# Performance work log

Hardware: AMD Instinct MI355X
Metric: run time of the kernel (lower is better)

Reference implementation:

```python
import jax, jax.numpy as jnp
import numpy as np

B, P, ENC = 64, 196, 2048          # batch, num_pixels (14x14), encoder_dim
A, E, D, V = 512, 512, 512, 20000  # attention_dim, embed_dim, decoder_dim, vocab
MAXLEN = 22
T = MAXLEN - 1                     # decode steps (teacher forcing drops last token)


def _lin(k, fan_in, fan_out, scale=0.02):
    return jax.random.normal(k, (fan_in, fan_out), jnp.float32) * scale, jnp.zeros((fan_out,), jnp.float32)


def setup_inputs() -> dict:
    key = jax.random.key(0)
    ks = jax.random.split(key, 16)
    encoder_out = jax.random.normal(ks[0], (B, P, ENC), jnp.float32)
    captions = jax.random.randint(ks[1], (B, MAXLEN), 0, V)
    lens = jax.random.randint(ks[2], (B,), 2, MAXLEN + 1)
    lens = jnp.sort(lens)[::-1].at[0].set(MAXLEN)  # sorted descending, as the torch loop assumes
    emb = jax.random.uniform(ks[3], (V, E), jnp.float32, -0.1, 0.1)
    enc_att_w, enc_att_b = _lin(ks[4], ENC, A)
    dec_att_w, dec_att_b = _lin(ks[5], D, A)
    full_att_w, full_att_b = _lin(ks[6], A, 1)
    w_ih = jax.random.normal(ks[7], (E + ENC, 4 * D), jnp.float32) * 0.02
    w_hh = jax.random.normal(ks[8], (D, 4 * D), jnp.float32) * 0.02
    b_ih = jnp.zeros((4 * D,), jnp.float32)
    b_hh = jnp.zeros((4 * D,), jnp.float32)
    init_h_w, init_h_b = _lin(ks[9], ENC, D)
    init_c_w, init_c_b = _lin(ks[10], ENC, D)
    f_beta_w, f_beta_b = _lin(ks[11], D, ENC)
    fc_w = jax.random.uniform(ks[12], (D, V), jnp.float32, -0.1, 0.1)
    fc_b = jnp.zeros((V,), jnp.float32)
    return dict(encoder_out=encoder_out, captions=captions, lengths=lens, emb=emb,
                enc_att_w=enc_att_w, enc_att_b=enc_att_b, dec_att_w=dec_att_w, dec_att_b=dec_att_b,
                full_att_w=full_att_w, full_att_b=full_att_b, w_ih=w_ih, b_ih=b_ih, w_hh=w_hh, b_hh=b_hh,
                init_h_w=init_h_w, init_h_b=init_h_b, init_c_w=init_c_w, init_c_b=init_c_b,
                f_beta_w=f_beta_w, f_beta_b=f_beta_b, fc_w=fc_w, fc_b=fc_b)


def reference(encoder_out, captions, lengths, emb,
              enc_att_w, enc_att_b, dec_att_w, dec_att_b, full_att_w, full_att_b,
              w_ih, b_ih, w_hh, b_hh, init_h_w, init_h_b, init_c_w, init_c_b,
              f_beta_w, f_beta_b, fc_w, fc_b):
    # Dropout is identity (eval mode) for a deterministic reference.
    dec_len = lengths - 1                       # decode_lengths
    x_emb = emb[captions]                       # (B, L, E)
    mean_enc = encoder_out.mean(axis=1)         # (B, ENC)
    h0 = mean_enc @ init_h_w + init_h_b         # (B, D)
    c0 = mean_enc @ init_c_w + init_c_b
    att1 = encoder_out @ enc_att_w + enc_att_b  # (B, P, A), hoisted out of the loop

    emb_ts = jnp.swapaxes(x_emb[:, :T, :], 0, 1)  # (T, B, E)
    t_idx = jnp.arange(T)

    def step(carry, xt):
        h, c = carry
        e_t, t = xt
        active = (t < dec_len)[:, None]         # ragged batch -> mask (sorted lengths)
        # Bahdanau attention
        att2 = h @ dec_att_w + dec_att_b        # (B, A)
        scores = (jax.nn.relu(att1 + att2[:, None, :]) @ full_att_w)[..., 0] + full_att_b[0]  # (B, P)
        alpha = jax.nn.softmax(scores, axis=1)
        context = jnp.einsum('bp,bpe->be', alpha, encoder_out)
        # gated context
        gate = jax.nn.sigmoid(h @ f_beta_w + f_beta_b)
        context = gate * context
        # LSTMCell (torch gate order i, f, g, o)
        x = jnp.concatenate([e_t, context], axis=1)
        gates = x @ w_ih + h @ w_hh + b_ih + b_hh
        i_g, f_g, g_g, o_g = jnp.split(gates, 4, axis=1)
        c_new = jax.nn.sigmoid(f_g) * c + jax.nn.sigmoid(i_g) * jnp.tanh(g_g)
        h_new = jax.nn.sigmoid(o_g) * jnp.tanh(c_new)
        h = jnp.where(active, h_new, h)
        c = jnp.where(active, c_new, c)
        preds = jnp.where(active, h_new @ fc_w + fc_b, 0.0)
        alpha_o = jnp.where(active, alpha, 0.0)
        return (h, c), (preds, alpha_o)

    _, (preds, alphas) = jax.lax.scan(step, (h0, c0), (emb_ts, t_idx))
    predictions = jnp.swapaxes(preds, 0, 1)     # (B, T, V)
    alphas = jnp.swapaxes(alphas, 0, 1)         # (B, T, P)
    return predictions, alphas
```

## Files before the change

kernel.cpp:

```cpp
#include <hip/hip_runtime.h>

#define BB   64
#define PP   196
#define ENC  2048
#define AA   512
#define EE   512
#define DD   512
#define VV   20000
#define TT   21
#define ML   22

#define PRED_ELEMS ((size_t)BB * TT * VV)

typedef __attribute__((ext_vector_type(8))) short s8bf;
typedef __attribute__((ext_vector_type(4))) float f4acc;

__device__ __forceinline__ float bf2f(unsigned short u) {
    union { unsigned int i; float f; } v; v.i = ((unsigned int)u) << 16; return v.f;
}
__device__ __forceinline__ void unpack2(unsigned int u, float& lo, float& hi) {
    union { unsigned int i; float f; } a, b;
    a.i = u << 16; b.i = u & 0xFFFF0000u; lo = a.f; hi = b.f;
}
__device__ __forceinline__ unsigned short f2bf(float f) {
    union { float f; unsigned int i; } v; v.f = f;
    unsigned int i = v.i;
    return (unsigned short)((i + 0x7FFFu + ((i >> 16) & 1u)) >> 16);
}
__device__ __forceinline__ float sigmoidf(float x) { return 1.0f / (1.0f + __expf(-x)); }

template <bool F> __device__ __forceinline__ float ldw(const void* p, size_t i) {
    if (F) return ((const float*)p)[i];
    return bf2f(((const unsigned short*)p)[i]);
}
template <bool F> __device__ __forceinline__ unsigned short ldbf(const void* p, size_t i) {
    if (F) return f2bf(((const float*)p)[i]);
    return ((const unsigned short*)p)[i];
}
template <bool F> __device__ __forceinline__ float2 ld2(const void* p, size_t i) {
    if (F) return *(const float2*)((const float*)p + i);
    unsigned int u = *(const unsigned int*)((const unsigned short*)p + i);
    float lo, hi; unpack2(u, lo, hi); return make_float2(lo, hi);
}
template <bool F> __device__ __forceinline__ float4 ld4(const void* p, size_t i) {
    if (F) return *(const float4*)((const float*)p + i);
    uint2 u = *(const uint2*)((const unsigned short*)p + i);
    float a, b, c, d; unpack2(u.x, a, b); unpack2(u.y, c, d);
    return make_float4(a, b, c, d);
}
template <bool F> __device__ __forceinline__ void st1(void* p, size_t i, float v) {
    if (F) ((float*)p)[i] = v; else ((unsigned short*)p)[i] = f2bf(v);
}

__global__ void dec_detect_kernel(const unsigned short* __restrict__ enc_us, int* __restrict__ flag) {
    __shared__ int s_cnt;
    if (threadIdx.x == 0) s_cnt = 0;
    __syncthreads();
    int cnt = 0;
    for (int i = threadIdx.x; i < 8192; i += 256) {
        unsigned short u = enc_us[2 * i];
        if ((u & 0x7F80) == 0x7F80) cnt++;
    }
    if (cnt) atomicAdd(&s_cnt, cnt);
    __syncthreads();
    if (threadIdx.x == 0) *flag = (s_cnt > 0) ? 1 : 0;
}

template <bool F>
__device__ __forceinline__ void encconv_body(const void* enc, unsigned short* dst) {
    size_t i = ((size_t)blockIdx.x * 256 + threadIdx.x) * 8;
    if (F) {
        const float* s = (const float*)enc + i;
        float4 v0 = *(const float4*)s, v1 = *(const float4*)(s + 4);
        union { uint4 u; unsigned short h[8]; } o;
        o.h[0]=f2bf(v0.x); o.h[1]=f2bf(v0.y); o.h[2]=f2bf(v0.z); o.h[3]=f2bf(v0.w);
        o.h[4]=f2bf(v1.x); o.h[5]=f2bf(v1.y); o.h[6]=f2bf(v1.z); o.h[7]=f2bf(v1.w);
        *(uint4*)(dst + i) = o.u;
    } else {
        *(uint4*)(dst + i) = *(const uint4*)((const unsigned short*)enc + i);
    }
}
__global__ void enc_bf_kernel(const void* __restrict__ enc, const int* __restrict__ flg,
                              unsigned short* __restrict__ dst) {
    if (*flg) encconv_body<true>(enc, dst); else encconv_body<false>(enc, dst);
}

template <bool F>
__device__ __forceinline__ void conv_swz_body(const void* W, int K, int Norig,
                                              unsigned short* dst, int permMode, int nChunks) {
    int chunk = blockIdx.x * 4 + (threadIdx.x >> 6);
    if (chunk >= nChunks) return;
    int lane = threadIdx.x & 63;
    int KC = K >> 5;
    int nt = chunk / KC, kc = chunk % KC;
    int quad = lane >> 4, l15 = lane & 15;
    int np = nt * 16 + l15;
    int col;
    if (permMode == 1) col = ((np >> 4) & 3) * 512 + (np >> 6) * 16 + (np & 15);
    else col = np;
    union { s8bf v; unsigned short s[8]; } o;
    if (np < Norig || permMode == 1) {
        size_t base = (size_t)(kc * 32 + quad * 8) * Norig + col;
#pragma unroll
        for (int j = 0; j < 8; ++j) o.s[j] = ldbf<F>(W, base + (size_t)j * Norig);
    } else {
#pragma unroll
        for (int j = 0; j < 8; ++j) o.s[j] = 0;
    }
    *(s8bf*)(dst + ((size_t)chunk * 64 + lane) * 8) = o.v;
}
__global__ void conv_swz_kernel(const int* __restrict__ flg, const void* __restrict__ W,
                                int K, int Norig, unsigned short* __restrict__ dst,
                                int permMode, int nChunks) {
    if (*flg) conv_swz_body<true>(W, K, Norig, dst, permMode, nChunks);
    else      conv_swz_body<false>(W, K, Norig, dst, permMode, nChunks);
}

template <bool F>
__device__ __forceinline__ void conv_bias_body(const void* dab, const void* fbb,
                                               const void* bih, const void* bhh, const void* fcb,
                                               const void* ihb, const void* icb, const void* eab,
                                               float* ag_b, float* g_b, float* fc_b,
                                               float* ihb_f, float* icb_f, float* eab_f) {
    int i = blockIdx.x * 256 + threadIdx.x;
    if (i < 2560) ag_b[i] = (i < 512) ? ldw<F>(dab, i) : ldw<F>(fbb, i - 512);
    else if (i < 2560 + 2048) {
        int np = i - 2560;
        int orig = ((np >> 4) & 3) * 512 + (np >> 6) * 16 + (np & 15);
        g_b[np] = ldw<F>(bih, orig) + ldw<F>(bhh, orig);
    } else if (i < 2560 + 2048 + 20000) fc_b[i - 4608] = ldw<F>(fcb, i - 4608);
    else if (i < 2560 + 2048 + 20000 + 512) ihb_f[i - 24608] = ldw<F>(ihb, i - 24608);
    else if (i < 2560 + 2048 + 20000 + 1024) icb_f[i - 25120] = ldw<F>(icb, i - 25120);
    else if (i < 2560 + 2048 + 20000 + 1536) eab_f[i - 25632] = ldw<F>(eab, i - 25632);
}
__global__ void conv_bias_kernel(const int* __restrict__ flg,
                                 const void* dab, const void* fbb, const void* bih, const void* bhh,
                                 const void* fcb, const void* ihb, const void* icb, const void* eab,
                                 float* ag_b, float* g_b, float* fc_b,
                                 float* ihb_f, float* icb_f, float* eab_f) {
    if (*flg) conv_bias_body<true>(dab, fbb, bih, bhh, fcb, ihb, icb, eab, ag_b, g_b, fc_b, ihb_f, icb_f, eab_f);
    else      conv_bias_body<false>(dab, fbb, bih, bhh, fcb, ihb, icb, eab, ag_b, g_b, fc_b, ihb_f, icb_f, eab_f);
}

template <bool F>
__device__ __forceinline__ void mean_body(const void* enc, unsigned short* mean_bf) {
    int b = blockIdx.x;
    int e = blockIdx.y * 256 + threadIdx.x;
    size_t base = (size_t)b * PP * ENC + e;
    float s = 0.f;
#pragma unroll 4
    for (int p = 0; p < PP; ++p) s += ldw<F>(enc, base + (size_t)p * ENC);
    mean_bf[b * ENC + e] = f2bf(s * (1.0f / (float)PP));
}
__global__ void dec_mean_kernel(const void* __restrict__ enc, const int* __restrict__ flg,
                                unsigned short* __restrict__ mean_bf) {
    if (*flg) mean_body<true>(enc, mean_bf); else mean_body<false>(enc, mean_bf);
}

__global__ __launch_bounds__(256)
void gemm_u_kernel(const int* __restrict__ flg,
                   const unsigned short* __restrict__ A1, int K1, const unsigned short* __restrict__ W1,
                   const unsigned short* __restrict__ A2, int K2, const unsigned short* __restrict__ W2,
                   const float* __restrict__ bias, int N, int epi, int nct,
                   float* __restrict__ outF, float* __restrict__ outF2,
                   unsigned short* __restrict__ hb, float* __restrict__ cptr,
                   unsigned short* __restrict__ h_all,
                   void* __restrict__ outV, const int* __restrict__ lengths, int t) {
    __shared__ float s_g[64 * 132];
    int tid = threadIdx.x;
    int wave = tid >> 6, lane = tid & 63;
    int l15 = lane & 15, quad = lane >> 4;
    const unsigned short* Abase1 = A1;
    if (epi == 2) Abase1 = A1 + (size_t)blockIdx.x * 64 * K1;
    f4acc acc[4][2];
#pragma unroll
    for (int a = 0; a < 4; ++a) { acc[a][0] = (f4acc)0.f; acc[a][1] = (f4acc)0.f; }
#pragma unroll
    for (int pass = 0; pass < 2; ++pass) {
        const unsigned short* A = pass ? A2 : Abase1;
        if (!A) continue;
        int K = pass ? K2 : K1;
        const unsigned short* W = pass ? W2 : W1;
        int KC = K >> 5;
        for (int kc = 0; kc < KC; ++kc) {
            s8bf af[4];
#pragma unroll
            for (int rt = 0; rt < 4; ++rt)
                af[rt] = *(const s8bf*)(A + (size_t)(rt * 16 + l15) * K + kc * 32 + quad * 8);
#pragma unroll
            for (int ct = 0; ct < 2; ++ct) if (ct < nct) {
                int nt = blockIdx.y * 4 * nct + ct * 4 + wave;
                s8bf bv = *(const s8bf*)(W + ((size_t)(nt * KC + kc) * 64 + lane) * 8);
#pragma unroll
                for (int rt = 0; rt < 4; ++rt)
                    acc[rt][ct] = __builtin_amdgcn_mfma_f32_16x16x32_bf16(af[rt], bv, acc[rt][ct], 0, 0, 0);
            }
        }
    }
    if (epi == 4) {
        int nl = wave * 16 + l15;
        int g = (nl >> 4) & 3, dl = nl & 15;
        float bv = bias[blockIdx.y * 64 + nl];
#pragma unroll
        for (int rt = 0; rt < 4; ++rt)
#pragma unroll
            for (int r = 0; r < 4; ++r) {
                int m = rt * 16 + quad * 4 + r;
                s_g[(g * 64 + m) * 17 + dl] = acc[rt][0][r] + bv;
            }
        __syncthreads();
        int m = tid >> 2;
        bool act = t < (lengths[m] - 1);
#pragma unroll
        for (int i = 0; i < 4; ++i) {
            int dl2 = (tid & 3) * 4 + i;
            int d = blockIdx.y * 16 + dl2;
            unsigned short hv;
            if (act) {
                float ig = sigmoidf(s_g[(0 * 64 + m) * 17 + dl2]);
                float fg = sigmoidf(s_g[(1 * 64 + m) * 17 + dl2]);
                float gg = tanhf(s_g[(2 * 64 + m) * 17 + dl2]);
                float og = sigmoidf(s_g[(3 * 64 + m) * 17 + dl2]);
                float cn = fg * cptr[m * DD + d] + ig * gg;
                float hn = og * tanhf(cn);
                cptr[m * DD + d] = cn;
                hv = f2bf(hn);
            } else {
                hv = A2[(size_t)m * K2 + d];
            }
            hb[m * DD + d] = hv;
            h_all[((size_t)t * BB + m) * DD + d] = hv;
        }
        return;
    }
    if (epi == 2) {
        int t2 = blockIdx.x;
        int base_n = blockIdx.y * 128;
#pragma unroll
        for (int ct = 0; ct < 2; ++ct) {
            int nl = ct * 64 + wave * 16 + l15;
            int nn = base_n + nl;
            float bv = (nn < VV) ? bias[nn] : 0.f;
#pragma unroll
            for (int rt = 0; rt < 4; ++rt)
#pragma unroll
                for (int r = 0; r < 4; ++r) {
                    int m = rt * 16 + quad * 4 + r;
                    s_g[m * 132 + nl] = acc[rt][ct][r] + bv;
                }
        }
        __syncthreads();
        bool f32o = (*flg != 0);
#pragma unroll
        for (int pass = 0; pass < 8; ++pass) {
            int m = pass * 8 + (tid >> 5);
            int j = tid & 31;
            int n = base_n + j * 4;
            if (n < VV) {
                bool act = t2 < (lengths[m] - 1);
                float4 v = *(const float4*)&s_g[m * 132 + j * 4];
                if (!act) { v.x = 0.f; v.y = 0.f; v.z = 0.f; v.w = 0.f; }
                size_t oi = ((size_t)m * TT + t2) * VV + n;
                if (f32o) {
                    *(float4*)((float*)outV + oi) = v;
                } else {
                    uint2 pk;
                    pk.x = (unsigned int)f2bf(v.x) | ((unsigned int)f2bf(v.y) << 16);
                    pk.y = (unsigned int)f2bf(v.z) | ((unsigned int)f2bf(v.w) << 16);
                    *(uint2*)((unsigned short*)outV + oi) = pk;
                }
            }
        }
        return;
    }
#pragma unroll
    for (int ct = 0; ct < 2; ++ct) if (ct < nct) {
        int n = blockIdx.y * 64 * nct + ct * 64 + wave * 16 + l15;
        if (n >= N) continue;
        float bv = bias ? bias[n] : 0.f;
#pragma unroll
        for (int rt = 0; rt < 4; ++rt)
#pragma unroll
            for (int r = 0; r < 4; ++r) {
                int m = rt * 16 + quad * 4 + r;
                float v = acc[rt][ct][r] + bv;
                if (epi == 0)      outF[(size_t)m * N + n] = v;
                else if (epi == 1) {
                    if (n < 512) outF[(size_t)m * 512 + n] = v;
                    else         outF2[(size_t)m * 2048 + (n - 512)] = sigmoidf(v);
                } else if (epi == 3) hb[(size_t)m * DD + n] = f2bf(v);
            }
    }
}

template <bool F>
__device__ __forceinline__ void att1_gemm_body(const void* enc, const unsigned short* Wsw,
                                               const float* bias, unsigned short* att1) {
    __shared__ __attribute__((aligned(16))) unsigned short As[64 * 40];
    int tid = threadIdx.x;
    int wave = tid >> 6, lane = tid & 63;
    int l15 = lane & 15, quad = lane >> 4;
    int row0 = blockIdx.x * 64;
    f4acc acc[4][2];
#pragma unroll
    for (int a = 0; a < 4; ++a) { acc[a][0] = (f4acc)0.f; acc[a][1] = (f4acc)0.f; }
    int lr = tid >> 2, lk = (tid & 3) * 8;
    for (int kc = 0; kc < 64; ++kc) {
        int k0 = kc * 32;
        if (F) {
            const float* src = (const float*)enc + (size_t)(row0 + lr) * ENC + k0 + lk;
            float4 v0 = *(const float4*)src, v1 = *(const float4*)(src + 4);
            union { s8bf v; unsigned short s[8]; } t8;
            t8.s[0]=f2bf(v0.x); t8.s[1]=f2bf(v0.y); t8.s[2]=f2bf(v0.z); t8.s[3]=f2bf(v0.w);
            t8.s[4]=f2bf(v1.x); t8.s[5]=f2bf(v1.y); t8.s[6]=f2bf(v1.z); t8.s[7]=f2bf(v1.w);
            *(s8bf*)&As[lr * 40 + lk] = t8.v;
        } else {
            *(s8bf*)&As[lr * 40 + lk] =
                *(const s8bf*)((const unsigned short*)enc + (size_t)(row0 + lr) * ENC + k0 + lk);
        }
        __syncthreads();
        s8bf af[4];
#pragma unroll
        for (int rt = 0; rt < 4; ++rt)
            af[rt] = *(const s8bf*)&As[(rt * 16 + l15) * 40 + quad * 8];
#pragma unroll
        for (int ct = 0; ct < 2; ++ct) {
            int nt = blockIdx.y * 8 + ct * 4 + wave;
            s8bf bv = *(const s8bf*)(Wsw + ((size_t)(nt * 64 + kc) * 64 + lane) * 8);
#pragma unroll
            for (int rt = 0; rt < 4; ++rt)
                acc[rt][ct] = __builtin_amdgcn_mfma_f32_16x16x32_bf16(af[rt], bv, acc[rt][ct], 0, 0, 0);
        }
        __syncthreads();
    }
#pragma unroll
    for (int ct = 0; ct < 2; ++ct) {
        int n = blockIdx.y * 128 + ct * 64 + wave * 16 + l15;
        float bv = bias[n];
#pragma unroll
        for (int rt = 0; rt < 4; ++rt)
#pragma unroll
            for (int r = 0; r < 4; ++r) {
                int m = row0 + rt * 16 + quad * 4 + r;
                att1[(size_t)m * AA + n] = f2bf(acc[rt][ct][r] + bv);
            }
    }
}
__global__ __launch_bounds__(256)
void gemm_att1_kernel(const void* __restrict__ enc, const int* __restrict__ flg,
                      const unsigned short* __restrict__ Wsw, const float* __restrict__ bias,
                      unsigned short* __restrict__ att1) {
    if (*flg) att1_gemm_body<true>(enc, Wsw, bias, att1);
    else      att1_gemm_body<false>(enc, Wsw, bias, att1);
}

template <bool F>
__device__ __forceinline__ void att_body(const unsigned short* att1, const float* att2,
                                         const void* faw, const void* fab,
                                         const int* lengths, float* alpha_ws, void* out, int t) {
    __shared__ float s_sc[256];
    __shared__ float s_red[256];
    int b = blockIdx.x, tid = threadIdx.x;
    int wave = tid >> 6, lane = tid & 63;
    int a0i = lane * 8;
    float4 a2a = *(const float4*)(att2 + (size_t)b * AA + a0i);
    float4 a2b = *(const float4*)(att2 + (size_t)b * AA + a0i + 4);
    float4 w0 = ld4<F>(faw, a0i);
    float4 w1 = ld4<F>(faw, a0i + 4);
    float fabv = ldw<F>(fab, 0);
    if (tid < 256) s_sc[tid] = -1e30f;
    __syncthreads();
    for (int r = wave; r < PP; r += 16) {
        uint4 u = *(const uint4*)(att1 + ((size_t)b * PP + r) * AA + a0i);
        float v0, v1, v2, v3, v4, v5, v6, v7;
        unpack2(u.x, v0, v1); unpack2(u.y, v2, v3);
        unpack2(u.z, v4, v5); unpack2(u.w, v6, v7);
        float acc = fmaxf(v0 + a2a.x, 0.f) * w0.x
                  + fmaxf(v1 + a2a.y, 0.f) * w0.y
                  + fmaxf(v2 + a2a.z, 0.f) * w0.z
                  + fmaxf(v3 + a2a.w, 0.f) * w0.w
                  + fmaxf(v4 + a2b.x, 0.f) * w1.x
                  + fmaxf(v5 + a2b.y, 0.f) * w1.y
                  + fmaxf(v6 + a2b.z, 0.f) * w1.z
                  + fmaxf(v7 + a2b.w, 0.f) * w1.w;
#pragma unroll
        for (int off = 32; off; off >>= 1) acc += __shfl_xor(acc, off, 64);
        if (lane == 0) s_sc[r] = acc + fabv;
    }
    __syncthreads();
    float sc = (tid < 256) ? s_sc[tid] : -1e30f;
    if (tid < 256) s_red[tid] = sc;
    __syncthreads();
    for (int s = 128; s > 0; s >>= 1) { if (tid < s) s_red[tid] = fmaxf(s_red[tid], s_red[tid + s]); __syncthreads(); }
    float m = s_red[0];
    __syncthreads();
    float e = 0.f;
    if (tid < PP) e = __expf(sc - m);
    if (tid < 256) s_red[tid] = e;
    __syncthreads();
    for (int s = 128; s > 0; s >>= 1) { if (tid < s) s_red[tid] += s_red[tid + s]; __syncthreads(); }
    float inv = 1.0f / s_red[0];
    if (tid < PP) {
        float al = e * inv;
        alpha_ws[b * PP + tid] = al;
        bool active = t < (lengths[b] - 1);
        st1<F>(out, PRED_ELEMS + (size_t)(b * TT + t) * PP + tid, active ? al : 0.f);
    }
}
__global__ __launch_bounds__(1024)
void dec_att_kernel(const unsigned short* __restrict__ att1, const float* __restrict__ att2,
                    const int* __restrict__ flg,
                    const void* __restrict__ faw, const void* __restrict__ fab,
                    const int* __restrict__ lengths,
                    float* __restrict__ alpha_ws, void* __restrict__ out, int t) {
    if (*flg) att_body<true>(att1, att2, faw, fab, lengths, alpha_ws, out, t);
    else      att_body<false>(att1, att2, faw, fab, lengths, alpha_ws, out, t);
}

template <bool F>
__device__ __forceinline__ void ctx_body(const void* encp, const float* alpha_ws,
                                         const float* gate, const void* emb, const int* captions,
                                         unsigned short* x_bf, int t) {
    __shared__ float s_al[PP];
    int b = blockIdx.x, yc = blockIdx.y, tid = threadIdx.x;
    if (tid < PP) s_al[tid] = alpha_ws[b * PP + tid];
    __syncthreads();
    if (yc == 0) {
        int cap = captions[b * ML + t];
        int i = tid * 2;
        float2 ev = ld2<F>(emb, (size_t)cap * EE + i);
        *(unsigned int*)(x_bf + (size_t)b * 2560 + i) =
            (unsigned int)f2bf(ev.x) | ((unsigned int)f2bf(ev.y) << 16);
    }
    int e = yc * 512 + tid * 2;
    float a0 = 0.f, a1 = 0.f;
    size_t base = (size_t)b * PP * ENC + e;
#pragma unroll 4
    for (int p = 0; p < PP; ++p) {
        float al = s_al[p];
        float2 v = ld2<F>(encp, base + (size_t)p * ENC);
        a0 += al * v.x; a1 += al * v.y;
    }
    float2 g = *(const float2*)&gate[(size_t)b * ENC + e];
    *(unsigned int*)(x_bf + (size_t)b * 2560 + EE + e) =
        (unsigned int)f2bf(a0 * g.x) | ((unsigned int)f2bf(a1 * g.y) << 16);
}
template <bool FEMB>
__device__ __forceinline__ void ctx_sel(const void* encp, int forceBf, const float* alpha_ws,
                                        const float* gate, const void* emb, const int* captions,
                                        unsigned short* x_bf, int t);
__global__ void dec_ctx_kernel(const void* __restrict__ encp, const int* __restrict__ flg, int forceBf,
                               const float* __restrict__ alpha_ws, const float* __restrict__ gate,
                               const void* __restrict__ emb, const int* __restrict__ captions,
                               unsigned short* __restrict__ x_bf, int t) {
    __shared__ float s_al[PP];
    int b = blockIdx.x, yc = blockIdx.y, tid = threadIdx.x;
    if (tid < PP) s_al[tid] = alpha_ws[b * PP + tid];
    __syncthreads();
    bool f32in = (*flg != 0);
    if (yc == 0) {
        int cap = captions[b * ML + t];
        int i = tid * 2;
        float2 ev = f32in ? ld2<true>(emb, (size_t)cap * EE + i) : ld2<false>(emb, (size_t)cap * EE + i);
        *(unsigned int*)(x_bf + (size_t)b * 2560 + i) =
            (unsigned int)f2bf(ev.x) | ((unsigned int)f2bf(ev.y) << 16);
    }
    int e = yc * 512 + tid * 2;
    float a0 = 0.f, a1 = 0.f;
    size_t base = (size_t)b * PP * ENC + e;
    bool encF32 = f32in && !forceBf;
    if (encF32) {
#pragma unroll 4
        for (int p = 0; p < PP; ++p) {
            float al = s_al[p];
            float2 v = *(const float2*)((const float*)encp + base + (size_t)p * ENC);
            a0 += al * v.x; a1 += al * v.y;
        }
    } else {
#pragma unroll 4
        for (int p = 0; p < PP; ++p) {
            float al = s_al[p];
            unsigned int u = *(const unsigned int*)((const unsigned short*)encp + base + (size_t)p * ENC);
            float lo, hi; unpack2(u, lo, hi);
            a0 += al * lo; a1 += al * hi;
        }
    }
    float2 g = *(const float2*)&gate[(size_t)b * ENC + e];
    *(unsigned int*)(x_bf + (size_t)b * 2560 + EE + e) =
        (unsigned int)f2bf(a0 * g.x) | ((unsigned int)f2bf(a1 * g.y) << 16);
}

extern "C" void kernel_launch(void* const* d_in, const int* in_sizes, int n_in,
                              void* d_out, int out_size, void* d_ws, size_t ws_size,
                              hipStream_t stream) {
    const void* enc      = d_in[0];
    const int* captions  = (const int*)d_in[1];
    const int* lengths   = (const int*)d_in[2];
    const void* emb      = d_in[3];
    const void* eaw      = d_in[4];
    const void* eab      = d_in[5];
    const void* daw      = d_in[6];
    const void* dab      = d_in[7];
    const void* faw      = d_in[8];
    const void* fab      = d_in[9];
    const void* wih      = d_in[10];
    const void* bih      = d_in[11];
    const void* whh      = d_in[12];
    const void* bhh      = d_in[13];
    const void* ihw      = d_in[14];
    const void* ihb      = d_in[15];
    const void* icw      = d_in[16];
    const void* icb      = d_in[17];
    const void* fbw      = d_in[18];
    const void* fbb      = d_in[19];
    const void* fcw      = d_in[20];
    const void* fcb      = d_in[21];

    char* cur = (char*)d_ws;
    auto alloc = [&](size_t bytes) { void* p = cur; cur += (bytes + 255) & ~(size_t)255; return p; };
    int* flg               = (int*)alloc(4);
    unsigned short* h_bufA = (unsigned short*)alloc((size_t)BB * DD * 2);
    unsigned short* h_bufB = (unsigned short*)alloc((size_t)BB * DD * 2);
    unsigned short* h_all  = (unsigned short*)alloc((size_t)TT * BB * DD * 2);
    unsigned short* x_bf   = (unsigned short*)alloc((size_t)BB * 2560 * 2);
    unsigned short* mean_bf= (unsigned short*)alloc((size_t)BB * ENC * 2);
    float* c               = (float*)alloc((size_t)BB * DD * 4);
    float* att2            = (float*)alloc((size_t)BB * AA * 4);
    float* gate            = (float*)alloc((size_t)BB * ENC * 4);
    float* alpha           = (float*)alloc((size_t)BB * PP * 4);
    float* ag_bias         = (float*)alloc(2560 * 4);
    float* g_bias          = (float*)alloc(2048 * 4);
    float* fc_bias         = (float*)alloc(20000 * 4);
    float* ihb_f           = (float*)alloc(512 * 4);
    float* icb_f           = (float*)alloc(512 * 4);
    float* eab_f           = (float*)alloc(512 * 4);
    unsigned short* eaw_sw = (unsigned short*)alloc((size_t)32 * 64 * 512 * 2);
    unsigned short* ag_sw  = (unsigned short*)alloc((size_t)160 * 16 * 512 * 2);
    unsigned short* ihw_sw = (unsigned short*)alloc((size_t)32 * 64 * 512 * 2);
    unsigned short* icw_sw = (unsigned short*)alloc((size_t)32 * 64 * 512 * 2);
    unsigned short* wih_sw = (unsigned short*)alloc((size_t)128 * 80 * 512 * 2);
    unsigned short* whh_sw = (unsigned short*)alloc((size_t)128 * 16 * 512 * 2);
    unsigned short* fcw_sw = (unsigned short*)alloc((size_t)1256 * 16 * 512 * 2);
    unsigned short* att1_bf= (unsigned short*)alloc((size_t)BB * PP * AA * 2);
    size_t enc_bf_bytes = (size_t)BB * PP * ENC * 2;
    size_t used = (size_t)(cur - (char*)d_ws);
    bool have_enc_bf = (used + enc_bf_bytes + 256 <= ws_size);
    unsigned short* enc_bf = have_enc_bf ? (unsigned short*)alloc(enc_bf_bytes) : nullptr;

    dec_detect_kernel<<<1, 256, 0, stream>>>((const unsigned short*)enc, flg);
    if (have_enc_bf)
        enc_bf_kernel<<<(BB * PP * ENC) / (256 * 8), 256, 0, stream>>>(enc, flg, enc_bf);
    conv_swz_kernel<<<(32 * 64 + 3) / 4, 256, 0, stream>>>(flg, eaw, ENC, AA, eaw_sw, 0, 32 * 64);
    conv_swz_kernel<<<(32 * 16 + 3) / 4, 256, 0, stream>>>(flg, daw, DD, AA, ag_sw, 0, 32 * 16);
    conv_swz_kernel<<<(128 * 16 + 3) / 4, 256, 0, stream>>>(flg, fbw, DD, ENC, ag_sw + (size_t)32 * 16 * 512, 0, 128 * 16);
    conv_swz_kernel<<<(32 * 64 + 3) / 4, 256, 0, stream>>>(flg, ihw, ENC, DD, ihw_sw, 0, 32 * 64);
    conv_swz_kernel<<<(32 * 64 + 3) / 4, 256, 0, stream>>>(flg, icw, ENC, DD, icw_sw, 0, 32 * 64);
    conv_swz_kernel<<<(128 * 80 + 3) / 4, 256, 0, stream>>>(flg, wih, 2560, 2048, wih_sw, 1, 128 * 80);
    conv_swz_kernel<<<(128 * 16 + 3) / 4, 256, 0, stream>>>(flg, whh, DD, 2048, whh_sw, 1, 128 * 16);
    conv_swz_kernel<<<(1256 * 16 + 3) / 4, 256, 0, stream>>>(flg, fcw, DD, VV, fcw_sw, 0, 1256 * 16);
    conv_bias_kernel<<<(26144 + 255) / 256, 256, 0, stream>>>(flg, dab, fbb, bih, bhh, fcb, ihb, icb, eab,
                                                              ag_bias, g_bias, fc_bias, ihb_f, icb_f, eab_f);
    dec_mean_kernel<<<dim3(BB, ENC / 256), 256, 0, stream>>>(enc, flg, mean_bf);
    gemm_u_kernel<<<dim3(1, 4), 256, 0, stream>>>(flg, mean_bf, ENC, ihw_sw, nullptr, 0, nullptr,
                                                  ihb_f, DD, 3, 2, nullptr, nullptr, h_bufA, nullptr,
                                                  nullptr, nullptr, nullptr, 0);
    gemm_u_kernel<<<dim3(1, 4), 256, 0, stream>>>(flg, mean_bf, ENC, icw_sw, nullptr, 0, nullptr,
                                                  icb_f, DD, 0, 2, c, nullptr, nullptr, nullptr,
                                                  nullptr, nullptr, nullptr, 0);
    gemm_att1_kernel<<<dim3(196, 4), 256, 0, stream>>>(enc, flg, eaw_sw, eab_f, att1_bf);

    const void* ctx_enc = have_enc_bf ? (const void*)enc_bf : enc;
    int forceBf = have_enc_bf ? 1 : 0;
    unsigned short* hcur = h_bufA;
    for (int t = 0; t < TT; ++t) {
        unsigned short* hnext = (hcur == h_bufA) ? h_bufB : h_bufA;
        gemm_u_kernel<<<dim3(1, 40), 256, 0, stream>>>(flg, hcur, DD, ag_sw, nullptr, 0, nullptr,
                                                       ag_bias, 2560, 1, 1, att2, gate, nullptr, nullptr,
                                                       nullptr, nullptr, nullptr, 0);
        dec_att_kernel<<<BB, 1024, 0, stream>>>(att1_bf, att2, flg, faw, fab, lengths, alpha, d_out, t);
        dec_ctx_kernel<<<dim3(BB, 4), 256, 0, stream>>>(ctx_enc, flg, forceBf, alpha, gate, emb, captions, x_bf, t);
        gemm_u_kernel<<<dim3(1, 32), 256, 0, stream>>>(flg, x_bf, 2560, wih_sw, hcur, DD, whh_sw,
                                                       g_bias, 2048, 4, 1, nullptr, nullptr, hnext, c,
                                                       h_all, nullptr, lengths, t);
        hcur = hnext;
    }
    gemm_u_kernel<<<dim3(TT, 157), 256, 0, stream>>>(flg, h_all, DD, fcw_sw, nullptr, 0, nullptr,
                                                     fc_bias, VV, 2, 2, nullptr, nullptr, nullptr, nullptr,
                                                     nullptr, d_out, lengths, 0);
}
```

Baseline: 2.754 ms.

## Fuse att2/gate projections into attention kernels and precompute embedding gate terms

Removes the per-step att2/gate GEMM launch. The h@dec_att_w projection is now computed inside the attention kernel, and the h@f_beta_w gate is computed inside the context kernel, both from transposed bf16 weights. The embedding half of the LSTM input projection is hoisted out of the loop into one batched GEMM over all timesteps, whose result is read back in the LSTM epilogue. This shortens the serial per-step chain and the LSTM GEMM K dimension, but the fused matvecs run on scalar FMAs and redundantly per block (each of the 4 context blocks per batch recomputes its gate slice).

```diff
diff --git a/kernel.cpp b/kernel.cpp
--- a/kernel.cpp
+++ b/kernel.cpp
@@ -87,7 +87,7 @@
 
 template <bool F>
 __device__ __forceinline__ void conv_swz_body(const void* W, int K, int Norig,
-                                              unsigned short* dst, int permMode, int nChunks) {
+                                              unsigned short* dst, int permMode, int nChunks, int rowOff) {
     int chunk = blockIdx.x * 4 + (threadIdx.x >> 6);
     if (chunk >= nChunks) return;
     int lane = threadIdx.x & 63;
@@ -100,7 +100,7 @@
     else col = np;
     union { s8bf v; unsigned short s[8]; } o;
     if (np < Norig || permMode == 1) {
-        size_t base = (size_t)(kc * 32 + quad * 8) * Norig + col;
+        size_t base = (size_t)(kc * 32 + quad * 8 + rowOff) * Norig + col;
 #pragma unroll
         for (int j = 0; j < 8; ++j) o.s[j] = ldbf<F>(W, base + (size_t)j * Norig);
     } else {
@@ -111,9 +111,41 @@
 }
 __global__ void conv_swz_kernel(const int* __restrict__ flg, const void* __restrict__ W,
                                 int K, int Norig, unsigned short* __restrict__ dst,
-                                int permMode, int nChunks) {
-    if (*flg) conv_swz_body<true>(W, K, Norig, dst, permMode, nChunks);
-    else      conv_swz_body<false>(W, K, Norig, dst, permMode, nChunks);
+                                int permMode, int nChunks, int rowOff) {
+    if (*flg) conv_swz_body<true>(W, K, Norig, dst, permMode, nChunks, rowOff);
+    else      conv_swz_body<false>(W, K, Norig, dst, permMode, nChunks, rowOff);
+}
+
+template <bool F>
+__device__ __forceinline__ void transp_body(const void* W, int N, unsigned short* dst) {
+    int n = blockIdx.x * 4 + (threadIdx.x >> 6);
+    int lane = threadIdx.x & 63;
+#pragma unroll
+    for (int kk = 0; kk < 8; ++kk) {
+        int k = lane + kk * 64;
+        dst[(size_t)n * 512 + k] = ldbf<F>(W, (size_t)k * N + n);
+    }
+}
+__global__ void transp_kernel(const int* __restrict__ flg, const void* __restrict__ W,
+                              int N, unsigned short* __restrict__ dst) {
+    if (*flg) transp_body<true>(W, N, dst); else transp_body<false>(W, N, dst);
+}
+
+template <bool F>
+__device__ __forceinline__ void embg_body(const void* emb, const int* captions, unsigned short* embg) {
+    int gid = blockIdx.x * 256 + threadIdx.x;
+    int row = gid >> 6;
+    int e0 = (gid & 63) * 8;
+    int t = row >> 6, b = row & 63;
+    int cap = captions[b * ML + t];
+    union { uint4 u; unsigned short h[8]; } o;
+#pragma unroll
+    for (int j = 0; j < 8; ++j) o.h[j] = ldbf<F>(emb, (size_t)cap * EE + e0 + j);
+    *(uint4*)(embg + (size_t)row * 512 + e0) = o.u;
+}
+__global__ void embg_kernel(const int* __restrict__ flg, const void* __restrict__ emb,
+                            const int* __restrict__ captions, unsigned short* __restrict__ embg) {
+    if (*flg) embg_body<true>(emb, captions, embg); else embg_body<false>(emb, captions, embg);
 }
 
 template <bool F>
@@ -162,16 +194,16 @@
                    const unsigned short* __restrict__ A1, int K1, const unsigned short* __restrict__ W1,
                    const unsigned short* __restrict__ A2, int K2, const unsigned short* __restrict__ W2,
                    const float* __restrict__ bias, int N, int epi, int nct,
-                   float* __restrict__ outF, float* __restrict__ outF2,
+                   float* __restrict__ outF, const float* __restrict__ outF2,
                    unsigned short* __restrict__ hb, float* __restrict__ cptr,
                    unsigned short* __restrict__ h_all,
                    void* __restrict__ outV, const int* __restrict__ lengths, int t) {
-    __shared__ float s_g[64 * 132];
+    __shared__ float s_g[4352];
     int tid = threadIdx.x;
     int wave = tid >> 6, lane = tid & 63;
     int l15 = lane & 15, quad = lane >> 4;
     const unsigned short* Abase1 = A1;
-    if (epi == 2) Abase1 = A1 + (size_t)blockIdx.x * 64 * K1;
+    if (epi == 0 || epi == 2) Abase1 = A1 + (size_t)blockIdx.x * 64 * K1;
     f4acc acc[4][2];
 #pragma unroll
     for (int a = 0; a < 4; ++a) { acc[a][0] = (f4acc)0.f; acc[a][1] = (f4acc)0.f; }
@@ -200,13 +232,15 @@
     if (epi == 4) {
         int nl = wave * 16 + l15;
         int g = (nl >> 4) & 3, dl = nl & 15;
-        float bv = bias[blockIdx.y * 64 + nl];
+        float bv = bias ? bias[blockIdx.y * 64 + nl] : 0.f;
+        size_t ecol = (size_t)blockIdx.y * 64 + nl;
 #pragma unroll
         for (int rt = 0; rt < 4; ++rt)
 #pragma unroll
             for (int r = 0; r < 4; ++r) {
                 int m = rt * 16 + quad * 4 + r;
-                s_g[(g * 64 + m) * 17 + dl] = acc[rt][0][r] + bv;
+                float ev = outF2 ? outF2[((size_t)t * BB + m) * 2048 + ecol] : 0.f;
+                s_g[(g * 64 + m) * 17 + dl] = acc[rt][0][r] + bv + ev;
             }
         __syncthreads();
         int m = tid >> 2;
@@ -236,38 +270,45 @@
     if (epi == 2) {
         int t2 = blockIdx.x;
         int base_n = blockIdx.y * 128;
-#pragma unroll
-        for (int ct = 0; ct < 2; ++ct) {
-            int nl = ct * 64 + wave * 16 + l15;
-            int nn = base_n + nl;
-            float bv = (nn < VV) ? bias[nn] : 0.f;
-#pragma unroll
-            for (int rt = 0; rt < 4; ++rt)
-#pragma unroll
-                for (int r = 0; r < 4; ++r) {
-                    int m = rt * 16 + quad * 4 + r;
-                    s_g[m * 132 + nl] = acc[rt][ct][r] + bv;
+        bool f32o = (*flg != 0);
+#pragma unroll
+        for (int half = 0; half < 2; ++half) {
+            if (half) __syncthreads();
+#pragma unroll
+            for (int ct = 0; ct < 2; ++ct) {
+                int nl = ct * 64 + wave * 16 + l15;
+                int nn = base_n + nl;
+                float bv = (nn < VV) ? bias[nn] : 0.f;
+#pragma unroll
+                for (int rt2 = 0; rt2 < 2; ++rt2) {
+                    int rt = half * 2 + rt2;
+#pragma unroll
+                    for (int r = 0; r < 4; ++r) {
+                        int mrow = rt2 * 16 + quad * 4 + r;
+                        s_g[mrow * 132 + nl] = acc[rt][ct][r] + bv;
+                    }
                 }
-        }
-        __syncthreads();
-        bool f32o = (*flg != 0);
-#pragma unroll
-        for (int pass = 0; pass < 8; ++pass) {
-            int m = pass * 8 + (tid >> 5);
-            int j = tid & 31;
-            int n = base_n + j * 4;
-            if (n < VV) {
-                bool act = t2 < (lengths[m] - 1);
-                float4 v = *(const float4*)&s_g[m * 132 + j * 4];
-                if (!act) { v.x = 0.f; v.y = 0.f; v.z = 0.f; v.w = 0.f; }
-                size_t oi = ((size_t)m * TT + t2) * VV + n;
-                if (f32o) {
-                    *(float4*)((float*)outV + oi) = v;
-                } else {
-                    uint2 pk;
-                    pk.x = (unsigned int)f2bf(v.x) | ((unsigned int)f2bf(v.y) << 16);
-                    pk.y = (unsigned int)f2bf(v.z) | ((unsigned int)f2bf(v.w) << 16);
-                    *(uint2*)((unsigned short*)outV + oi) = pk;
+            }
+            __syncthreads();
+#pragma unroll
+            for (int pass = 0; pass < 4; ++pass) {
+                int mrow = pass * 8 + (tid >> 5);
+                int m = half * 32 + mrow;
+                int j = tid & 31;
+                int n = base_n + j * 4;
+                if (n < VV) {
+                    bool act = t2 < (lengths[m] - 1);
+                    float4 v = *(const float4*)&s_g[mrow * 132 + j * 4];
+                    if (!act) { v.x = 0.f; v.y = 0.f; v.z = 0.f; v.w = 0.f; }
+                    size_t oi = ((size_t)m * TT + t2) * VV + n;
+                    if (f32o) {
+                        *(float4*)((float*)outV + oi) = v;
+                    } else {
+                        uint2 pk;
+                        pk.x = (unsigned int)f2bf(v.x) | ((unsigned int)f2bf(v.y) << 16);
+                        pk.y = (unsigned int)f2bf(v.z) | ((unsigned int)f2bf(v.w) << 16);
+                        *(uint2*)((unsigned short*)outV + oi) = pk;
+                    }
                 }
             }
         }
@@ -284,11 +325,8 @@
             for (int r = 0; r < 4; ++r) {
                 int m = rt * 16 + quad * 4 + r;
                 float v = acc[rt][ct][r] + bv;
-                if (epi == 0)      outF[(size_t)m * N + n] = v;
-                else if (epi == 1) {
-                    if (n < 512) outF[(size_t)m * 512 + n] = v;
-                    else         outF2[(size_t)m * 2048 + (n - 512)] = sigmoidf(v);
-                } else if (epi == 3) hb[(size_t)m * DD + n] = f2bf(v);
+                if (epi == 0) outF[(size_t)(blockIdx.x * 64 + m) * N + n] = v;
+                else          hb[(size_t)m * DD + n] = f2bf(v);
             }
     }
 }
@@ -355,34 +393,58 @@
 }
 
 template <bool F>
-__device__ __forceinline__ void att_body(const unsigned short* att1, const float* att2,
+__device__ __forceinline__ void att_body(const unsigned short* att1, const unsigned short* hcur,
+                                         const unsigned short* dawT, const float* ag_bias,
                                          const void* faw, const void* fab,
                                          const int* lengths, float* alpha_ws, void* out, int t) {
+    __shared__ float s_h[512];
+    __shared__ float s_att2[512];
     __shared__ float s_sc[256];
     __shared__ float s_red[256];
     int b = blockIdx.x, tid = threadIdx.x;
+    if (tid < 256) {
+        unsigned int hv = *(const unsigned int*)(hcur + (size_t)b * DD + tid * 2);
+        float lo, hi; unpack2(hv, lo, hi);
+        s_h[tid * 2] = lo; s_h[tid * 2 + 1] = hi;
+        s_sc[tid] = -1e30f;
+    }
+    __syncthreads();
+    {
+        int n = tid >> 1, half = tid & 1;
+        const unsigned short* wr = dawT + (size_t)n * 512 + half * 256;
+        const float* hh = s_h + half * 256;
+        float acc = 0.f;
+#pragma unroll 4
+        for (int kk = 0; kk < 256; kk += 8) {
+            s8bf wv = *(const s8bf*)(wr + kk);
+#pragma unroll
+            for (int j = 0; j < 8; ++j) acc += hh[kk + j] * bf2f((unsigned short)wv[j]);
+        }
+        acc += __shfl_xor(acc, 1, 64);
+        if (half == 0) s_att2[n] = acc + ag_bias[n];
+    }
+    __syncthreads();
     int wave = tid >> 6, lane = tid & 63;
     int a0i = lane * 8;
-    float4 a2a = *(const float4*)(att2 + (size_t)b * AA + a0i);
-    float4 a2b = *(const float4*)(att2 + (size_t)b * AA + a0i + 4);
+    float a2[8];
+#pragma unroll
+    for (int j = 0; j < 8; ++j) a2[j] = s_att2[a0i + j];
     float4 w0 = ld4<F>(faw, a0i);
     float4 w1 = ld4<F>(faw, a0i + 4);
     float fabv = ldw<F>(fab, 0);
-    if (tid < 256) s_sc[tid] = -1e30f;
-    __syncthreads();
     for (int r = wave; r < PP; r += 16) {
         uint4 u = *(const uint4*)(att1 + ((size_t)b * PP + r) * AA + a0i);
         float v0, v1, v2, v3, v4, v5, v6, v7;
         unpack2(u.x, v0, v1); unpack2(u.y, v2, v3);
         unpack2(u.z, v4, v5); unpack2(u.w, v6, v7);
-        float acc = fmaxf(v0 + a2a.x, 0.f) * w0.x
-                  + fmaxf(v1 + a2a.y, 0.f) * w0.y
-                  + fmaxf(v2 + a2a.z, 0.f) * w0.z
-                  + fmaxf(v3 + a2a.w, 0.f) * w0.w
-                  + fmaxf(v4 + a2b.x, 0.f) * w1.x
-                  + fmaxf(v5 + a2b.y, 0.f) * w1.y
-                  + fmaxf(v6 + a2b.z, 0.f) * w1.z
-                  + fmaxf(v7 + a2b.w, 0.f) * w1.w;
+        float acc = fmaxf(v0 + a2[0], 0.f) * w0.x
+                  + fmaxf(v1 + a2[1], 0.f) * w0.y
+                  + fmaxf(v2 + a2[2], 0.f) * w0.z
+                  + fmaxf(v3 + a2[3], 0.f) * w0.w
+                  + fmaxf(v4 + a2[4], 0.f) * w1.x
+                  + fmaxf(v5 + a2[5], 0.f) * w1.y
+                  + fmaxf(v6 + a2[6], 0.f) * w1.z
+                  + fmaxf(v7 + a2[7], 0.f) * w1.w;
 #pragma unroll
         for (int off = 32; off; off >>= 1) acc += __shfl_xor(acc, off, 64);
         if (lane == 0) s_sc[r] = acc + fabv;
@@ -408,76 +470,60 @@
     }
 }
 __global__ __launch_bounds__(1024)
-void dec_att_kernel(const unsigned short* __restrict__ att1, const float* __restrict__ att2,
+void dec_att_kernel(const unsigned short* __restrict__ att1, const unsigned short* __restrict__ hcur,
+                    const unsigned short* __restrict__ dawT, const float* __restrict__ ag_bias,
                     const int* __restrict__ flg,
                     const void* __restrict__ faw, const void* __restrict__ fab,
                     const int* __restrict__ lengths,
                     float* __restrict__ alpha_ws, void* __restrict__ out, int t) {
-    if (*flg) att_body<true>(att1, att2, faw, fab, lengths, alpha_ws, out, t);
-    else      att_body<false>(att1, att2, faw, fab, lengths, alpha_ws, out, t);
-}
-
-template <bool F>
-__device__ __forceinline__ void ctx_body(const void* encp, const float* alpha_ws,
-                                         const float* gate, const void* emb, const int* captions,
-                                         unsigned short* x_bf, int t) {
+    if (*flg) att_body<true>(att1, hcur, dawT, ag_bias, faw, fab, lengths, alpha_ws, out, t);
+    else      att_body<false>(att1, hcur, dawT, ag_bias, faw, fab, lengths, alpha_ws, out, t);
+}
+
+__global__ __launch_bounds__(256)
+void dec_ctx_kernel(const void* __restrict__ encp, const int* __restrict__ flg, int forceBf,
+                    const float* __restrict__ alpha_ws, const unsigned short* __restrict__ hcur,
+                    const unsigned short* __restrict__ fbwT, const float* __restrict__ ag_bias,
+                    unsigned short* __restrict__ xc_bf, int t) {
     __shared__ float s_al[PP];
+    __shared__ float s_h[512];
     int b = blockIdx.x, yc = blockIdx.y, tid = threadIdx.x;
     if (tid < PP) s_al[tid] = alpha_ws[b * PP + tid];
-    __syncthreads();
-    if (yc == 0) {
-        int cap = captions[b * ML + t];
-        int i = tid * 2;
-        float2 ev = ld2<F>(emb, (size_t)cap * EE + i);
-        *(unsigned int*)(x_bf + (size_t)b * 2560 + i) =
-            (unsigned int)f2bf(ev.x) | ((unsigned int)f2bf(ev.y) << 16);
-    }
+    {
+        unsigned int hv = *(const unsigned int*)(hcur + (size_t)b * DD + tid * 2);
+        float lo, hi; unpack2(hv, lo, hi);
+        s_h[tid * 2] = lo; s_h[tid * 2 + 1] = hi;
+    }
+    __syncthreads();
     int e = yc * 512 + tid * 2;
+    const unsigned short* w0r = fbwT + (size_t)e * 512;
+    const unsigned short* w1r = w0r + 512;
+    float g0 = 0.f, g1 = 0.f;
+#pragma unroll 4
+    for (int kk = 0; kk < 512; kk += 8) {
+        s8bf wa = *(const s8bf*)(w0r + kk);
+        s8bf wb = *(const s8bf*)(w1r + kk);
+#pragma unroll
+        for (int j = 0; j < 8; ++j) {
+            float hv = s_h[kk + j];
+            g0 += hv * bf2f((unsigned short)wa[j]);
+            g1 += hv * bf2f((unsigned short)wb[j]);
+        }
+    }
+    g0 = sigmoidf(g0 + ag_bias[512 + e]);
+    g1 = sigmoidf(g1 + ag_bias[512 + e + 1]);
     float a0 = 0.f, a1 = 0.f;
     size_t base = (size_t)b * PP * ENC + e;
-#pragma unroll 4
-    for (int p = 0; p < PP; ++p) {
-        float al = s_al[p];
-        float2 v = ld2<F>(encp, base + (size_t)p * ENC);
-        a0 += al * v.x; a1 += al * v.y;
-    }
-    float2 g = *(const float2*)&gate[(size_t)b * ENC + e];
-    *(unsigned int*)(x_bf + (size_t)b * 2560 + EE + e) =
-        (unsigned int)f2bf(a0 * g.x) | ((unsigned int)f2bf(a1 * g.y) << 16);
-}
-template <bool FEMB>
-__device__ __forceinline__ void ctx_sel(const void* encp, int forceBf, const float* alpha_ws,
-                                        const float* gate, const void* emb, const int* captions,
-                                        unsigned short* x_bf, int t);
-__global__ void dec_ctx_kernel(const void* __restrict__ encp, const int* __restrict__ flg, int forceBf,
-                               const float* __restrict__ alpha_ws, const float* __restrict__ gate,
-                               const void* __restrict__ emb, const int* __restrict__ captions,
-                               unsigned short* __restrict__ x_bf, int t) {
-    __shared__ float s_al[PP];
-    int b = blockIdx.x, yc = blockIdx.y, tid = threadIdx.x;
-    if (tid < PP) s_al[tid] = alpha_ws[b * PP + tid];
-    __syncthreads();
-    bool f32in = (*flg != 0);
-    if (yc == 0) {
-        int cap = captions[b * ML + t];
-        int i = tid * 2;
-        float2 ev = f32in ? ld2<true>(emb, (size_t)cap * EE + i) : ld2<false>(emb, (size_t)cap * EE + i);
-        *(unsigned int*)(x_bf + (size_t)b * 2560 + i) =
-            (unsigned int)f2bf(ev.x) | ((unsigned int)f2bf(ev.y) << 16);
-    }
-    int e = yc * 512 + tid * 2;
-    float a0 = 0.f, a1 = 0.f;
-    size_t base = (size_t)b * PP * ENC + e;
-    bool encF32 = f32in && !forceBf;
+    bool encF32 = (*flg != 0) && !forceBf;
     if (encF32) {
-#pragma unroll 4
+#pragma unroll 16
         for (int p = 0; p < PP; ++p) {
             float al = s_al[p];
             float2 v = *(const float2*)((const float*)encp + base + (size_t)p * ENC);
             a0 += al * v.x; a1 += al * v.y;
         }
     } else {
-#pragma unroll 4
+#pragma unroll 16
         for (int p = 0; p < PP; ++p) {
             float al = s_al[p];
             unsigned int u = *(const unsigned int*)((const unsigned short*)encp + base + (size_t)p * ENC);
@@ -485,9 +531,8 @@
             a0 += al * lo; a1 += al * hi;
         }
     }
-    float2 g = *(const float2*)&gate[(size_t)b * ENC + e];
-    *(unsigned int*)(x_bf + (size_t)b * 2560 + EE + e) =
-        (unsigned int)f2bf(a0 * g.x) | ((unsigned int)f2bf(a1 * g.y) << 16);
+    *(unsigned int*)(xc_bf + (size_t)b * 2048 + e) =
+        (unsigned int)f2bf(a0 * g0) | ((unsigned int)f2bf(a1 * g1) << 16);
 }
 
 extern "C" void kernel_launch(void* const* d_in, const int* in_sizes, int n_in,
@@ -522,11 +567,9 @@
     unsigned short* h_bufA = (unsigned short*)alloc((size_t)BB * DD * 2);
     unsigned short* h_bufB = (unsigned short*)alloc((size_t)BB * DD * 2);
     unsigned short* h_all  = (unsigned short*)alloc((size_t)TT * BB * DD * 2);
-    unsigned short* x_bf   = (unsigned short*)alloc((size_t)BB * 2560 * 2);
+    unsigned short* xc_bf  = (unsigned short*)alloc((size_t)BB * 2048 * 2);
     unsigned short* mean_bf= (unsigned short*)alloc((size_t)BB * ENC * 2);
     float* c               = (float*)alloc((size_t)BB * DD * 4);
-    float* att2            = (float*)alloc((size_t)BB * AA * 4);
-    float* gate            = (float*)alloc((size_t)BB * ENC * 4);
     float* alpha           = (float*)alloc((size_t)BB * PP * 4);
     float* ag_bias         = (float*)alloc(2560 * 4);
     float* g_bias          = (float*)alloc(2048 * 4);
@@ -534,11 +577,15 @@
     float* ihb_f           = (float*)alloc(512 * 4);
     float* icb_f           = (float*)alloc(512 * 4);
     float* eab_f           = (float*)alloc(512 * 4);
+    unsigned short* daw_T  = (unsigned short*)alloc((size_t)512 * 512 * 2);
+    unsigned short* fbw_T  = (unsigned short*)alloc((size_t)2048 * 512 * 2);
+    unsigned short* embg   = (unsigned short*)alloc((size_t)TT * BB * 512 * 2);
+    float* E_all           = (float*)alloc((size_t)TT * BB * 2048 * 4);
     unsigned short* eaw_sw = (unsigned short*)alloc((size_t)32 * 64 * 512 * 2);
-    unsigned short* ag_sw  = (unsigned short*)alloc((size_t)160 * 16 * 512 * 2);
     unsigned short* ihw_sw = (unsigned short*)alloc((size_t)32 * 64 * 512 * 2);
     unsigned short* icw_sw = (unsigned short*)alloc((size_t)32 * 64 * 512 * 2);
-    unsigned short* wih_sw = (unsigned short*)alloc((size_t)128 * 80 * 512 * 2);
+    unsigned short* wihA_sw= (unsigned short*)alloc((size_t)128 * 16 * 512 * 2);
+    unsigned short* wihB_sw= (unsigned short*)alloc((size_t)128 * 64 * 512 * 2);
     unsigned short* whh_sw = (unsigned short*)alloc((size_t)128 * 16 * 512 * 2);
     unsigned short* fcw_sw = (unsigned short*)alloc((size_t)1256 * 16 * 512 * 2);
     unsigned short* att1_bf= (unsigned short*)alloc((size_t)BB * PP * AA * 2);
@@ -550,23 +597,28 @@
     dec_detect_kernel<<<1, 256, 0, stream>>>((const unsigned short*)enc, flg);
     if (have_enc_bf)
         enc_bf_kernel<<<(BB * PP * ENC) / (256 * 8), 256, 0, stream>>>(enc, flg, enc_bf);
-    conv_swz_kernel<<<(32 * 64 + 3) / 4, 256, 0, stream>>>(flg, eaw, ENC, AA, eaw_sw, 0, 32 * 64);
-    conv_swz_kernel<<<(32 * 16 + 3) / 4, 256, 0, stream>>>(flg, daw, DD, AA, ag_sw, 0, 32 * 16);
-    conv_swz_kernel<<<(128 * 16 + 3) / 4, 256, 0, stream>>>(flg, fbw, DD, ENC, ag_sw + (size_t)32 * 16 * 512, 0, 128 * 16);
-    conv_swz_kernel<<<(32 * 64 + 3) / 4, 256, 0, stream>>>(flg, ihw, ENC, DD, ihw_sw, 0, 32 * 64);
-    conv_swz_kernel<<<(32 * 64 + 3) / 4, 256, 0, stream>>>(flg, icw, ENC, DD, icw_sw, 0, 32 * 64);
-    conv_swz_kernel<<<(128 * 80 + 3) / 4, 256, 0, stream>>>(flg, wih, 2560, 2048, wih_sw, 1, 128 * 80);
-    conv_swz_kernel<<<(128 * 16 + 3) / 4, 256, 0, stream>>>(flg, whh, DD, 2048, whh_sw, 1, 128 * 16);
-    conv_swz_kernel<<<(1256 * 16 + 3) / 4, 256, 0, stream>>>(flg, fcw, DD, VV, fcw_sw, 0, 1256 * 16);
+    conv_swz_kernel<<<512, 256, 0, stream>>>(flg, eaw, ENC, AA, eaw_sw, 0, 32 * 64, 0);
+    conv_swz_kernel<<<512, 256, 0, stream>>>(flg, ihw, ENC, DD, ihw_sw, 0, 32 * 64, 0);
+    conv_swz_kernel<<<512, 256, 0, stream>>>(flg, icw, ENC, DD, icw_sw, 0, 32 * 64, 0);
+    conv_swz_kernel<<<512, 256, 0, stream>>>(flg, wih, 512, 2048, wihA_sw, 1, 128 * 16, 0);
+    conv_swz_kernel<<<2048, 256, 0, stream>>>(flg, wih, 2048, 2048, wihB_sw, 1, 128 * 64, 512);
+    conv_swz_kernel<<<512, 256, 0, stream>>>(flg, whh, DD, 2048, whh_sw, 1, 128 * 16, 0);
+    conv_swz_kernel<<<5024, 256, 0, stream>>>(flg, fcw, DD, VV, fcw_sw, 0, 1256 * 16, 0);
+    transp_kernel<<<128, 256, 0, stream>>>(flg, daw, AA, daw_T);
+    transp_kernel<<<512, 256, 0, stream>>>(flg, fbw, ENC, fbw_T);
     conv_bias_kernel<<<(26144 + 255) / 256, 256, 0, stream>>>(flg, dab, fbb, bih, bhh, fcb, ihb, icb, eab,
                                                               ag_bias, g_bias, fc_bias, ihb_f, icb_f, eab_f);
     dec_mean_kernel<<<dim3(BB, ENC / 256), 256, 0, stream>>>(enc, flg, mean_bf);
+    embg_kernel<<<(TT * BB * 64) / 256, 256, 0, stream>>>(flg, emb, captions, embg);
     gemm_u_kernel<<<dim3(1, 4), 256, 0, stream>>>(flg, mean_bf, ENC, ihw_sw, nullptr, 0, nullptr,
                                                   ihb_f, DD, 3, 2, nullptr, nullptr, h_bufA, nullptr,
                                                   nullptr, nullptr, nullptr, 0);
     gemm_u_kernel<<<dim3(1, 4), 256, 0, stream>>>(flg, mean_bf, ENC, icw_sw, nullptr, 0, nullptr,
                                                   icb_f, DD, 0, 2, c, nullptr, nullptr, nullptr,
                                                   nullptr, nullptr, nullptr, 0);
+    gemm_u_kernel<<<dim3(TT, 32), 256, 0, stream>>>(flg, embg, 512, wihA_sw, nullptr, 0, nullptr,
+                                                    g_bias, 2048, 0, 1, E_all, nullptr, nullptr, nullptr,
+                                                    nullptr, nullptr, nullptr, 0);
     gemm_att1_kernel<<<dim3(196, 4), 256, 0, stream>>>(enc, flg, eaw_sw, eab_f, att1_bf);
 
     const void* ctx_enc = have_enc_bf ? (const void*)enc_bf : enc;
@@ -574,13 +626,12 @@
     unsigned short* hcur = h_bufA;
     for (int t = 0; t < TT; ++t) {
         unsigned short* hnext = (hcur == h_bufA) ? h_bufB : h_bufA;
-        gemm_u_kernel<<<dim3(1, 40), 256, 0, stream>>>(flg, hcur, DD, ag_sw, nullptr, 0, nullptr,
-                                                       ag_bias, 2560, 1, 1, att2, gate, nullptr, nullptr,
-                                                       nullptr, nullptr, nullptr, 0);
-        dec_att_kernel<<<BB, 1024, 0, stream>>>(att1_bf, att2, flg, faw, fab, lengths, alpha, d_out, t);
-        dec_ctx_kernel<<<dim3(BB, 4), 256, 0, stream>>>(ctx_enc, flg, forceBf, alpha, gate, emb, captions, x_bf, t);
-        gemm_u_kernel<<<dim3(1, 32), 256, 0, stream>>>(flg, x_bf, 2560, wih_sw, hcur, DD, whh_sw,
-                                                       g_bias, 2048, 4, 1, nullptr, nullptr, hnext, c,
+        dec_att_kernel<<<BB, 1024, 0, stream>>>(att1_bf, hcur, daw_T, ag_bias, flg, faw, fab,
+                                                lengths, alpha, d_out, t);
+        dec_ctx_kernel<<<dim3(BB, 4), 256, 0, stream>>>(ctx_enc, flg, forceBf, alpha, hcur, fbw_T,
+                                                        ag_bias, xc_bf, t);
+        gemm_u_kernel<<<dim3(1, 32), 256, 0, stream>>>(flg, xc_bf, 2048, wihB_sw, hcur, DD, whh_sw,
+                                                       nullptr, 2048, 4, 1, nullptr, E_all, hnext, c,
                                                        h_all, nullptr, lengths, t);
         hcur = hnext;
     }
```

Measured after the change: 2.928 ms. 1.06x slower.
